# Kernel optimization log

Hardware: AMD Instinct MI355X
Metric: run time of the kernel (lower is better)

Reference implementation:

```python
import jax, jax.numpy as jnp
import numpy as np

B, S, P, D, H, L, DF, O = 8, 1024, 128, 256, 4, 4, 1024, 10
DH = D // H  # 64
EPS = 1e-5


def get_positional_embeddings(seq_len, d):
    i = np.arange(seq_len, dtype=np.float64)[:, None]
    j = np.arange(d, dtype=np.float64)[None, :]
    even = np.sin(i / 10000 ** (j / d))
    odd = np.cos(i / 10000 ** ((j - 1) / d))
    return jnp.asarray(np.where(j % 2 == 0, even, odd), dtype=jnp.float32)


def layernorm(x, g, b):
    m = jnp.mean(x, axis=-1, keepdims=True)
    v = jnp.mean(jnp.square(x - m), axis=-1, keepdims=True)
    return (x - m) * jax.lax.rsqrt(v + EPS) * g + b


def setup_inputs() -> dict:
    key = jax.random.key(0)
    ks = jax.random.split(key, 20)
    w = lambda k, shp: (jax.random.normal(k, shp, dtype=jnp.float32) * 0.02)
    return {
        "images": jax.random.normal(ks[0], (B, S, P), dtype=jnp.float32),
        "Wp": w(ks[1], (D, P)), "bp": jnp.zeros((D,), jnp.float32),
        "cls": jax.random.uniform(ks[2], (1, D), dtype=jnp.float32),
        "pos": get_positional_embeddings(S + 1, D),
        "ln1_g": jnp.ones((L, D), jnp.float32), "ln1_b": jnp.zeros((L, D), jnp.float32),
        "Wq": w(ks[3], (L, H, DH, DH)), "bq": jnp.zeros((L, H, DH), jnp.float32),
        "Wk": w(ks[4], (L, H, DH, DH)), "bk": jnp.zeros((L, H, DH), jnp.float32),
        "Wv": w(ks[5], (L, H, DH, DH)), "bv": jnp.zeros((L, H, DH), jnp.float32),
        "ln2_g": jnp.ones((L, D), jnp.float32), "ln2_b": jnp.zeros((L, D), jnp.float32),
        "W1": w(ks[6], (L, DF, D)), "b1": jnp.zeros((L, DF), jnp.float32),
        "W2": w(ks[7], (L, D, DF)), "b2": jnp.zeros((L, D), jnp.float32),
        "Wo": w(ks[8], (O, D)), "bo": jnp.zeros((O,), jnp.float32),
    }


def msa(x, Wq, bq, Wk, bk, Wv, bv):
    b, s, _ = x.shape
    xh = x.reshape(b, s, H, DH)  # split heads along feature dim
    # torch Linear: y = x @ W.T + b, per head
    q = jnp.einsum("bshd,hed->bhse", xh, Wq) + bq[None, :, None, :]
    k = jnp.einsum("bshd,hed->bhse", xh, Wk) + bk[None, :, None, :]
    v = jnp.einsum("bshd,hed->bhse", xh, Wv) + bv[None, :, None, :]
    scores = jnp.einsum("bhqd,bhkd->bhqk", q, k) / (DH ** 0.5)
    attn = jax.nn.softmax(scores, axis=-1)
    out = jnp.einsum("bhqk,bhkd->bhqd", attn, v)  # [b,h,s,dh]
    return out.transpose(0, 2, 1, 3).reshape(b, s, D)  # hstack heads


def reference(images, Wp, bp, cls, pos, ln1_g, ln1_b, Wq, bq, Wk, bk, Wv, bv,
              ln2_g, ln2_b, W1, b1, W2, b2, Wo, bo):
    tokens = jnp.einsum("bsp,dp->bsd", images, Wp) + bp
    x = jnp.concatenate([jnp.broadcast_to(cls[None], (B, 1, D)), tokens], axis=1)
    x = x + pos[None]
    for l in range(L):
        x = x + msa(layernorm(x, ln1_g[l], ln1_b[l]), Wq[l], bq[l], Wk[l], bk[l], Wv[l], bv[l])
        h = layernorm(x, ln2_g[l], ln2_b[l])
        h = jax.nn.gelu(jnp.einsum("bsd,fd->bsf", h, W1[l]) + b1[l], approximate=False)
        x = x + jnp.einsum("bsf,df->bsd", h, W2[l]) + b2[l]
    logits = x[:, 0] @ Wo.T + bo
    return jax.nn.softmax(logits, axis=-1)
```

## Files before the change

kernel.cpp:

```cpp
#include <hip/hip_runtime.h>
#include <hip/hip_bf16.h>
#include <cmath>

constexpr int B  = 8;
constexpr int S  = 1024;
constexpr int P  = 128;
constexpr int D  = 256;
constexpr int H  = 4;
constexpr int L  = 4;
constexpr int DF = 1024;
constexpr int O  = 10;
constexpr int DH = D / H;
constexpr int SP = S + 1;
constexpr int N  = B * SP;
constexpr int KVPAD = 1088;

typedef short bf16x8 __attribute__((ext_vector_type(8)));
typedef float f32x4 __attribute__((ext_vector_type(4)));
typedef float f32x16 __attribute__((ext_vector_type(16)));
typedef unsigned int u32;
typedef unsigned short u16;

static __device__ __forceinline__ u16 f2b(float f) {
    __hip_bfloat16 h = __float2bfloat16(f);
    u16 u; __builtin_memcpy(&u, &h, 2);
    return u;
}
static __device__ __forceinline__ float b2f(u16 u) {
    u32 uu = (u32)u << 16; float f; __builtin_memcpy(&f, &uu, 4);
    return f;
}
static __device__ __forceinline__ u32 pk2(float a, float b) {
    return (u32)f2b(a) | ((u32)f2b(b) << 16);
}
static __device__ __forceinline__ void gload_lds16(const void* g, void* l) {
    __builtin_amdgcn_global_load_lds((const __attribute__((address_space(1))) unsigned int*)g,
                                     (__attribute__((address_space(3))) unsigned int*)l, 16, 0, 0);
}

__global__ void cvt_all(const float* __restrict__ s0, u16* __restrict__ d0, int n0,
                        const float* __restrict__ s1, u16* __restrict__ d1, int n1,
                        const float* __restrict__ s2, u16* __restrict__ d2, int n2,
                        const float* __restrict__ s3, u16* __restrict__ d3, int n3) {
    int y = blockIdx.y;
    const float* s = y == 0 ? s0 : y == 1 ? s1 : y == 2 ? s2 : s3;
    u16* d = y == 0 ? d0 : y == 1 ? d1 : y == 2 ? d2 : d3;
    int n = y == 0 ? n0 : y == 1 ? n1 : y == 2 ? n2 : n3;
    int i = blockIdx.x * 256 + threadIdx.x;
    if (i < n) {
        float4 v = ((const float4*)s)[i];
        ushort4 o;
        o.x = f2b(v.x); o.y = f2b(v.y); o.z = f2b(v.z); o.w = f2b(v.w);
        ((ushort4*)d)[i] = o;
    }
}

__global__ void cls_kernel(const float* __restrict__ cls, const float* __restrict__ pos,
                           float* __restrict__ x) {
    int b = blockIdx.x, t = threadIdx.x;
    x[(size_t)b * SP * D + t] = cls[t] + pos[t];
}

__global__ void build_wqkv(const float* __restrict__ Wq, const float* __restrict__ bq,
                           const float* __restrict__ Wk, const float* __restrict__ bk,
                           const float* __restrict__ Wv, const float* __restrict__ bv,
                           u16* __restrict__ Wout, float* __restrict__ bout) {
    int r = blockIdx.x, l = blockIdx.y, c = threadIdx.x;
    int sec = r >> 8;
    int ef = r & 255, h = ef >> 6, e = ef & 63;
    const float* W  = sec == 0 ? Wq : sec == 1 ? Wk : Wv;
    const float* bi = sec == 0 ? bq : sec == 1 ? bk : bv;
    float scale = sec == 0 ? 0.125f * 1.4426950408889634f : 1.0f;
    float val = ((c >> 6) == h) ? W[(((size_t)l * H + h) * 64 + e) * 64 + (c & 63)] * scale : 0.f;
    Wout[((size_t)l * 768 + r) * 256 + c] = f2b(val);
    if (c == 0) bout[(size_t)l * 768 + r] = bi[((size_t)l * H + h) * 64 + e] * scale;
}

template <int EPI>
__global__ __launch_bounds__(256) void gemm_bf16(
        const u16* __restrict__ X, const u16* __restrict__ W,
        const float* __restrict__ bias, const float* __restrict__ pos,
        float* __restrict__ Yf, u16* __restrict__ Yb,
        int M, int F, int K, int kLen) {
    __shared__ u16 Al[2][64 * 64];
    __shared__ u16 Bl[2][128 * 64];
    const int t = threadIdx.x;
    const int m0 = blockIdx.y * 64, f0 = blockIdx.x * 128;
    const int w = t >> 6, l = t & 63;
    const int wm = w >> 1, wn = w & 1;
    const int q = l & 15, g = l >> 4;
    const int kOff = blockIdx.z * kLen;
    const int lr8 = l >> 3, lp = l & 7;

    f32x4 acc[2][4];
    const f32x4 zz = {0.f, 0.f, 0.f, 0.f};
#pragma unroll
    for (int i = 0; i < 2; ++i)
#pragma unroll
        for (int j = 0; j < 4; ++j) acc[i][j] = zz;

    auto stage = [&](int sb, int kbase) {
#pragma unroll
        for (int i = 0; i < 2; ++i) {
            int ca = w + 4 * i;
            int row = ca * 8 + lr8;
            int j = lp ^ (row & 7);
            gload_lds16(X + (size_t)(m0 + row) * K + kbase + j * 8, &Al[sb][ca * 512]);
        }
#pragma unroll
        for (int i = 0; i < 4; ++i) {
            int cb = w + 4 * i;
            int row = cb * 8 + lr8;
            int j = lp ^ (row & 7);
            gload_lds16(W + (size_t)(f0 + row) * K + kbase + j * 8, &Bl[sb][cb * 512]);
        }
    };

    const int nt = kLen / 64;
    stage(0, kOff);
    __syncthreads();
    int sb = 0;
    for (int ts = 0; ts < nt; ++ts) {
        if (ts + 1 < nt) stage(sb ^ 1, kOff + (ts + 1) * 64);
#pragma unroll
        for (int kk = 0; kk < 2; ++kk) {
            bf16x8 a[2], bfr[4];
#pragma unroll
            for (int fi = 0; fi < 2; ++fi) {
                int row = wm * 32 + fi * 16 + q;
                a[fi] = *(const bf16x8*)&Al[sb][row * 64 + (((kk * 4 + g) ^ (row & 7)) * 8)];
            }
#pragma unroll
            for (int fj = 0; fj < 4; ++fj) {
                int row = wn * 64 + fj * 16 + q;
                bfr[fj] = *(const bf16x8*)&Bl[sb][row * 64 + (((kk * 4 + g) ^ (row & 7)) * 8)];
            }
#pragma unroll
            for (int fi = 0; fi < 2; ++fi)
#pragma unroll
                for (int fj = 0; fj < 4; ++fj)
                    acc[fi][fj] = __builtin_amdgcn_mfma_f32_16x16x32_bf16(a[fi], bfr[fj], acc[fi][fj], 0, 0, 0);
        }
        __syncthreads();
        sb ^= 1;
    }

#pragma unroll
    for (int fi = 0; fi < 2; ++fi) {
#pragma unroll
        for (int r = 0; r < 4; ++r) {
            int m = m0 + wm * 32 + fi * 16 + g * 4 + r;
            if (m >= M) continue;
#pragma unroll
            for (int fj = 0; fj < 4; ++fj) {
                int f = f0 + wn * 64 + fj * 16 + q;
                float val = acc[fi][fj][r];
                if constexpr (EPI == 0) {
                    val += bias[f];
                    int s = m & 1023, bb = m >> 10;
                    size_t n = (size_t)bb * SP + s + 1;
                    Yf[n * D + f] = val + pos[(size_t)(s + 1) * D + f];
                } else if constexpr (EPI == 1) {
                    val += bias[f];
                    float gel = 0.5f * val * (1.0f + erff(val * 0.70710678118654752f));
                    Yb[(size_t)m * F + f] = f2b(gel);
                } else if constexpr (EPI == 2) {
                    val += bias[f];
                    Yf[(size_t)m * F + f] += val;
                } else if constexpr (EPI == 3) {
                    val += bias[f];
                    Yb[(size_t)m * F + f] = f2b(val);
                } else {
                    (Yf + (size_t)blockIdx.z * M * F)[(size_t)m * F + f] = val;
                }
            }
        }
    }
}

__global__ void transpose_v(const u16* __restrict__ qkv, u16* __restrict__ VTg) {
    __shared__ u16 tile[64][70];
    int bh = blockIdx.y, t0 = blockIdx.x * 64;
    int b = bh >> 2, h = bh & 3;
    int t = threadIdx.x;
    int r = t >> 3, c8 = (t & 7) * 8;
#pragma unroll
    for (int it = 0; it < 2; ++it) {
        int sp = t0 + it * 32 + r; if (sp > S) sp = S;
        uint4 v = *(const uint4*)(qkv + ((size_t)b * SP + sp) * 768 + 512 + h * 64 + c8);
        u32* dst = (u32*)&tile[it * 32 + r][c8];
        const u32* pv = (const u32*)&v;
#pragma unroll
        for (int k = 0; k < 4; ++k) dst[k] = pv[k];
    }
    __syncthreads();
#pragma unroll
    for (int it = 0; it < 2; ++it) {
        int d = it * 32 + (t >> 3);
        int spc = (t & 7) * 8;
        u16 tmp[8];
#pragma unroll
        for (int j = 0; j < 8; ++j) tmp[j] = tile[spc + j][d];
        *(uint4*)(VTg + ((size_t)bh * 64 + d) * KVPAD + t0 + spc) = *(const uint4*)tmp;
    }
}

__global__ void layernorm_bf16(const float* __restrict__ src,
                               const float* __restrict__ gw,
                               const float* __restrict__ bw,
                               u16* __restrict__ dst) {
    int row = blockIdx.x * 4 + (threadIdx.x >> 6);
    int l = threadIdx.x & 63;
    float4 v = *(const float4*)(src + (size_t)row * D + l * 4);
    float s = v.x + v.y + v.z + v.w;
    for (int off = 32; off; off >>= 1) s += __shfl_xor(s, off, 64);
    float mean = s * (1.0f / D);
    float dx0 = v.x - mean, dx1 = v.y - mean, dx2 = v.z - mean, dx3 = v.w - mean;
    float sq = dx0 * dx0 + dx1 * dx1 + dx2 * dx2 + dx3 * dx3;
    for (int off = 32; off; off >>= 1) sq += __shfl_xor(sq, off, 64);
    float rs = rsqrtf(sq * (1.0f / D) + 1e-5f);
    float4 gv = *(const float4*)(gw + l * 4);
    float4 bv = *(const float4*)(bw + l * 4);
    ushort4 o;
    o.x = f2b(dx0 * rs * gv.x + bv.x);
    o.y = f2b(dx1 * rs * gv.y + bv.y);
    o.z = f2b(dx2 * rs * gv.z + bv.z);
    o.w = f2b(dx3 * rs * gv.w + bv.w);
    *(ushort4*)(dst + (size_t)row * D + l * 4) = o;
}

__global__ __launch_bounds__(512, 4) void attn_stage(const u16* __restrict__ qkv,
                                                     const u16* __restrict__ VTg,
                                                     u16* __restrict__ opart,
                                                     float* __restrict__ lsum,
                                                     int nqt) {
    const int qg = blockIdx.x, bh = blockIdx.y, quarter = blockIdx.z;
    const int h4 = bh & 3, b = bh >> 2;
    const int t = threadIdx.x;
    const int wv = t >> 6, l = t & 63;
    const int col = l & 31, hh = l >> 5;

    __shared__ u16 Kl[5 * 64 * 64];
    __shared__ u16 Vl[5 * 64 * 64];

    const int kv_start = quarter * 256;
    const int kv_len = (quarter == 3) ? (SP - 768) : 256;
    const int ntiles = (kv_len + 63) >> 6;

    const int qt = qg * 8 + wv;
    const int q0w = qt * 32;

    bf16x8 qf[4];
    {
        int qr = q0w + col; if (qr > S) qr = S;
        const u16* qp = qkv + ((size_t)b * SP + qr) * 768 + h4 * 64 + hh * 8;
#pragma unroll
        for (int c = 0; c < 4; ++c) qf[c] = *(const bf16x8*)(qp + c * 16);
    }

    {
        const int rloc = wv * 8 + (l >> 3);
        const int j = (l & 7) ^ (((rloc >> 3) ^ rloc) & 7);
        for (int tt = 0; tt < ntiles; ++tt) {
            int krow = kv_start + tt * 64 + rloc; if (krow > S) krow = S;
            gload_lds16(qkv + ((size_t)b * SP + krow) * 768 + 256 + h4 * 64 + j * 8,
                        &Kl[(tt * 8 + wv) * 512]);
            gload_lds16(VTg + ((size_t)bh * 64 + rloc) * KVPAD + kv_start + tt * 64 + j * 8,
                        &Vl[(tt * 8 + wv) * 512]);
        }
    }
    __syncthreads();
    if (qt >= nqt) return;

    const int swA = ((col >> 3) ^ col) & 7;
    const int swB = swA ^ 4;

    f32x16 o0, o1;
#pragma unroll
    for (int r = 0; r < 16; ++r) { o0[r] = 0.f; o1[r] = 0.f; }
    float l_run = 0.f;

    for (int tile = 0; tile < ntiles; ++tile) {
        const int kv0 = tile * 64;
        const u16* Kt = &Kl[tile * 4096];
        const u16* Vt = &Vl[tile * 4096];

        f32x16 s0, s1;
#pragma unroll
        for (int r = 0; r < 16; ++r) { s0[r] = 0.f; s1[r] = 0.f; }
        __builtin_amdgcn_s_setprio(1);
#pragma unroll
        for (int c = 0; c < 4; ++c) {
            bf16x8 k0 = *(const bf16x8*)&Kt[col * 64 + (((2 * c + hh) ^ swA) * 8)];
            bf16x8 k1 = *(const bf16x8*)&Kt[(32 + col) * 64 + (((2 * c + hh) ^ swB) * 8)];
            s0 = __builtin_amdgcn_mfma_f32_32x32x16_bf16(k0, qf[c], s0, 0, 0, 0);
            s1 = __builtin_amdgcn_mfma_f32_32x32x16_bf16(k1, qf[c], s1, 0, 0, 0);
        }
        __builtin_amdgcn_s_setprio(0);

        float p[32];
#pragma unroll
        for (int r = 0; r < 16; ++r) { p[r] = s0[r]; p[16 + r] = s1[r]; }

        if (kv0 + 64 > kv_len) {
#pragma unroll
            for (int kvs = 0; kvs < 2; ++kvs)
#pragma unroll
                for (int r = 0; r < 16; ++r) {
                    int kvloc = kvs * 32 + (r & 3) + 8 * (r >> 2) + 4 * hh;
                    if (kv0 + kvloc >= kv_len) p[kvs * 16 + r] = -1e30f;
                }
        }

#pragma unroll
        for (int j = 0; j < 32; ++j) p[j] = exp2f(p[j]);
        {
            float t16[16];
#pragma unroll
            for (int j = 0; j < 16; ++j) t16[j] = p[2 * j] + p[2 * j + 1];
#pragma unroll
            for (int j = 0; j < 8; ++j) t16[j] = t16[j] + t16[j + 8];
#pragma unroll
            for (int j = 0; j < 4; ++j) t16[j] = t16[j] + t16[j + 4];
            l_run += (t16[0] + t16[1]) + (t16[2] + t16[3]);
        }

        __builtin_amdgcn_s_setprio(1);
#pragma unroll
        for (int kvs = 0; kvs < 2; ++kvs) {
            u32 pk[8];
#pragma unroll
            for (int i = 0; i < 8; ++i) pk[i] = pk2(p[kvs * 16 + 2 * i], p[kvs * 16 + 2 * i + 1]);
            u32 ex[4];
#pragma unroll
            for (int kk = 0; kk < 4; ++kk) {
                const int k = (kk < 2) ? kk : kk + 2;
                u32 send = hh ? pk[k] : pk[k + 2];
                ex[kk] = (u32)__shfl_xor((int)send, 32);
            }
#pragma unroll
            for (int cc = 0; cc < 2; ++cc) {
                union { u32 u[4]; bf16x8 v; } pa;
                u32 e0 = ex[cc * 2], e1 = ex[cc * 2 + 1];
                pa.u[0] = hh ? e0 : pk[4 * cc];
                pa.u[1] = hh ? e1 : pk[4 * cc + 1];
                pa.u[2] = hh ? pk[4 * cc + 2] : e0;
                pa.u[3] = hh ? pk[4 * cc + 3] : e1;
                int lch = kvs * 4 + cc * 2 + hh;
                bf16x8 v0 = *(const bf16x8*)&Vt[col * 64 + ((lch ^ swA) * 8)];
                bf16x8 v1 = *(const bf16x8*)&Vt[(32 + col) * 64 + ((lch ^ swB) * 8)];
                o0 = __builtin_amdgcn_mfma_f32_32x32x16_bf16(pa.v, v0, o0, 0, 0, 0);
                o1 = __builtin_amdgcn_mfma_f32_32x32x16_bf16(pa.v, v1, o1, 0, 0, 0);
            }
        }
        __builtin_amdgcn_s_setprio(0);
    }

    float l_full = l_run + __shfl_xor(l_run, 32);
    float inv = 1.0f / l_full;
    const size_t obase = ((size_t)quarter * 32 + bh) * SP;
#pragma unroll
    for (int r = 0; r < 16; ++r) {
        int qrow = (r & 3) + 8 * (r >> 2) + 4 * hh;
        float iv = __shfl(inv, qrow);
        int qq = q0w + qrow;
        if (qq < SP) {
            opart[(obase + qq) * 64 + col]      = f2b(o0[r] * iv);
            opart[(obase + qq) * 64 + 32 + col] = f2b(o1[r] * iv);
        }
    }
    if (l < 32) {
        int qq = q0w + l;
        if (qq < SP) lsum[obase + qq] = l_full;
    }
}

__global__ void combine_ln2(const u16* __restrict__ opart, const float* __restrict__ lsum,
                            const float* __restrict__ gw, const float* __restrict__ bw,
                            float* __restrict__ x, u16* __restrict__ lnb) {
    int row = blockIdx.x * 4 + (threadIdx.x >> 6);
    int l = threadIdx.x & 63;
    int b = row / SP, qq = row % SP;
    int h = l >> 4, d0 = (l * 4) & 63;
    int bh = b * 4 + h;
    float csum = 0.f, a0 = 0.f, a1 = 0.f, a2 = 0.f, a3 = 0.f;
#pragma unroll
    for (int i = 0; i < 4; ++i) {
        size_t idx = ((size_t)i * 32 + bh) * SP + qq;
        float c = lsum[idx];
        csum += c;
        ushort4 ov = *(const ushort4*)&opart[idx * 64 + d0];
        a0 += c * b2f(ov.x); a1 += c * b2f(ov.y); a2 += c * b2f(ov.z); a3 += c * b2f(ov.w);
    }
    float inv = 1.0f / csum;
    float4 xv = *(const float4*)(x + (size_t)row * D + l * 4);
    xv.x += a0 * inv; xv.y += a1 * inv; xv.z += a2 * inv; xv.w += a3 * inv;
    *(float4*)(x + (size_t)row * D + l * 4) = xv;

    float s = xv.x + xv.y + xv.z + xv.w;
    for (int off = 32; off; off >>= 1) s += __shfl_xor(s, off, 64);
    float mean = s * (1.0f / D);
    float dx0 = xv.x - mean, dx1 = xv.y - mean, dx2 = xv.z - mean, dx3 = xv.w - mean;
    float sq = dx0 * dx0 + dx1 * dx1 + dx2 * dx2 + dx3 * dx3;
    for (int off = 32; off; off >>= 1) sq += __shfl_xor(sq, off, 64);
    float rs = rsqrtf(sq * (1.0f / D) + 1e-5f);
    float4 gv = *(const float4*)(gw + l * 4);
    float4 bv = *(const float4*)(bw + l * 4);
    ushort4 o;
    o.x = f2b(dx0 * rs * gv.x + bv.x);
    o.y = f2b(dx1 * rs * gv.y + bv.y);
    o.z = f2b(dx2 * rs * gv.z + bv.z);
    o.w = f2b(dx3 * rs * gv.w + bv.w);
    *(ushort4*)(lnb + (size_t)row * D + l * 4) = o;
}

__global__ void combine2_ln1(const float* __restrict__ Pk, const float* __restrict__ b2,
                             const float* __restrict__ gw, const float* __restrict__ bw,
                             float* __restrict__ x, u16* __restrict__ lnb) {
    int row = blockIdx.x * 4 + (threadIdx.x >> 6);
    int l = threadIdx.x & 63;
    float4 p0 = ((const float4*)Pk)[(size_t)row * 64 + l];
    float4 p1 = ((const float4*)Pk)[(size_t)N * 64 + (size_t)row * 64 + l];
    float4 bv2 = *(const float4*)(b2 + l * 4);
    float4 xv = *(const float4*)(x + (size_t)row * D + l * 4);
    xv.x += p0.x + p1.x + bv2.x;
    xv.y += p0.y + p1.y + bv2.y;
    xv.z += p0.z + p1.z + bv2.z;
    xv.w += p0.w + p1.w + bv2.w;
    *(float4*)(x + (size_t)row * D + l * 4) = xv;

    float s = xv.x + xv.y + xv.z + xv.w;
    for (int off = 32; off; off >>= 1) s += __shfl_xor(s, off, 64);
    float mean = s * (1.0f / D);
    float dx0 = xv.x - mean, dx1 = xv.y - mean, dx2 = xv.z - mean, dx3 = xv.w - mean;
    float sq = dx0 * dx0 + dx1 * dx1 + dx2 * dx2 + dx3 * dx3;
    for (int off = 32; off; off >>= 1) sq += __shfl_xor(sq, off, 64);
    float rs = rsqrtf(sq * (1.0f / D) + 1e-5f);
    float4 gv = *(const float4*)(gw + l * 4);
    float4 bv = *(const float4*)(bw + l * 4);
    ushort4 o;
    o.x = f2b(dx0 * rs * gv.x + bv.x);
    o.y = f2b(dx1 * rs * gv.y + bv.y);
    o.z = f2b(dx2 * rs * gv.z + bv.z);
    o.w = f2b(dx3 * rs * gv.w + bv.w);
    *(ushort4*)(lnb + (size_t)row * D + l * 4) = o;
}

__global__ void combine_cls_ln2(const u16* __restrict__ opart, const float* __restrict__ lsum,
                                const float* __restrict__ x,
                                const float* __restrict__ gw, const float* __restrict__ bw,
                                float* __restrict__ x_cls, u16* __restrict__ lnb_cls) {
    int b = blockIdx.x * 4 + (threadIdx.x >> 6);
    int l = threadIdx.x & 63;
    int h = l >> 4, d0 = (l * 4) & 63;
    int bh = b * 4 + h;
    float csum = 0.f, a0 = 0.f, a1 = 0.f, a2 = 0.f, a3 = 0.f;
#pragma unroll
    for (int i = 0; i < 4; ++i) {
        size_t idx = ((size_t)i * 32 + bh) * SP;
        float c = lsum[idx];
        csum += c;
        ushort4 ov = *(const ushort4*)&opart[idx * 64 + d0];
        a0 += c * b2f(ov.x); a1 += c * b2f(ov.y); a2 += c * b2f(ov.z); a3 += c * b2f(ov.w);
    }
    float inv = 1.0f / csum;
    float4 xv = *(const float4*)(x + (size_t)b * SP * D + l * 4);
    xv.x += a0 * inv; xv.y += a1 * inv; xv.z += a2 * inv; xv.w += a3 * inv;
    *(float4*)(x_cls + (size_t)b * D + l * 4) = xv;

    float s = xv.x + xv.y + xv.z + xv.w;
    for (int off = 32; off; off >>= 1) s += __shfl_xor(s, off, 64);
    float mean = s * (1.0f / D);
    float dx0 = xv.x - mean, dx1 = xv.y - mean, dx2 = xv.z - mean, dx3 = xv.w - mean;
    float sq = dx0 * dx0 + dx1 * dx1 + dx2 * dx2 + dx3 * dx3;
    for (int off = 32; off; off >>= 1) sq += __shfl_xor(sq, off, 64);
    float rs = rsqrtf(sq * (1.0f / D) + 1e-5f);
    float4 gv = *(const float4*)(gw + l * 4);
    float4 bv = *(const float4*)(bw + l * 4);
    ushort4 o;
    o.x = f2b(dx0 * rs * gv.x + bv.x);
    o.y = f2b(dx1 * rs * gv.y + bv.y);
    o.z = f2b(dx2 * rs * gv.z + bv.z);
    o.w = f2b(dx3 * rs * gv.w + bv.w);
    *(ushort4*)(lnb_cls + (size_t)b * D + l * 4) = o;
}

__global__ void head_kernel(const float* __restrict__ xc,
                            const float* __restrict__ Wo,
                            const float* __restrict__ bo,
                            float* __restrict__ out) {
    __shared__ float logits[B][O];
    int t = threadIdx.x;
    if (t < B * O) {
        int b = t / O, o = t % O;
        const float* xr = xc + (size_t)b * D;
        float acc = bo[o];
        for (int d = 0; d < D; ++d) acc += xr[d] * Wo[(size_t)o * D + d];
        logits[b][o] = acc;
    }
    __syncthreads();
    if (t < B) {
        float mx = -1e30f;
        for (int o = 0; o < O; ++o) mx = fmaxf(mx, logits[t][o]);
        float s = 0.f, e[O];
        for (int o = 0; o < O; ++o) { e[o] = expf(logits[t][o] - mx); s += e[o]; }
        float inv = 1.0f / s;
        for (int o = 0; o < O; ++o) out[t * O + o] = e[o] * inv;
    }
}

extern "C" void kernel_launch(void* const* d_in, const int* in_sizes, int n_in,
                              void* d_out, int out_size, void* d_ws, size_t ws_size,
                              hipStream_t stream) {
    const float* images = (const float*)d_in[0];
    const float* Wp     = (const float*)d_in[1];
    const float* bp     = (const float*)d_in[2];
    const float* cls    = (const float*)d_in[3];
    const float* pos    = (const float*)d_in[4];
    const float* ln1_g  = (const float*)d_in[5];
    const float* ln1_b  = (const float*)d_in[6];
    const float* Wq     = (const float*)d_in[7];
    const float* bq     = (const float*)d_in[8];
    const float* Wk     = (const float*)d_in[9];
    const float* bk     = (const float*)d_in[10];
    const float* Wv     = (const float*)d_in[11];
    const float* bv     = (const float*)d_in[12];
    const float* ln2_g  = (const float*)d_in[13];
    const float* ln2_b  = (const float*)d_in[14];
    const float* W1     = (const float*)d_in[15];
    const float* b1     = (const float*)d_in[16];
    const float* W2     = (const float*)d_in[17];
    const float* b2     = (const float*)d_in[18];
    const float* Wo     = (const float*)d_in[19];
    const float* bo     = (const float*)d_in[20];
    float* out = (float*)d_out;

    auto align256 = [](size_t v) { return (v + 255) & ~(size_t)255; };
    char* p = (char*)d_ws;
    float* x      = (float*)p; p += align256((size_t)N * D * 4);
    u16* lnb      = (u16*)p;   p += align256((size_t)N * D * 2);
    u16* qkvbuf   = (u16*)p;   p += align256((size_t)(N + 64) * 768 * 2);
    char* midop   = p;         p += align256((size_t)N * DF * 2);
    float* Pk     = (float*)p; p += align256((size_t)2 * N * D * 4);
    float* lsum   = (float*)p; p += align256((size_t)4 * 32 * SP * 4);
    u16* VTg      = (u16*)p;   p += align256((size_t)32 * 64 * KVPAD * 2);
    u16* imgb     = (u16*)p;   p += align256((size_t)B * S * P * 2);
    u16* Wpb      = (u16*)p;   p += align256((size_t)D * P * 2);
    u16* W1b      = (u16*)p;   p += align256((size_t)L * DF * D * 2);
    u16* W2b      = (u16*)p;   p += align256((size_t)L * D * DF * 2);
    u16* Wqkvb    = (u16*)p;   p += align256((size_t)L * 768 * 256 * 2);
    float* bqkvf  = (float*)p; p += align256((size_t)L * 768 * 4);
    float* x_cls  = (float*)p; p += align256((size_t)64 * D * 4);
    u16* lnb_cls  = (u16*)p;   p += align256((size_t)64 * D * 2);
    u16* mid_cls  = (u16*)p;   p += align256((size_t)64 * DF * 2);
    u16* mid      = (u16*)midop;
    u16* opart    = (u16*)midop;

    cvt_all<<<dim3(1024, 4), 256, 0, stream>>>(
        images, imgb, B * S * P / 4,
        Wp, Wpb, D * P / 4,
        W1, W1b, L * DF * D / 4,
        W2, W2b, L * D * DF / 4);
    build_wqkv<<<dim3(768, L), 256, 0, stream>>>(Wq, bq, Wk, bk, Wv, bv, Wqkvb, bqkvf);

    gemm_bf16<0><<<dim3(2, 128, 1), 256, 0, stream>>>(
        imgb, Wpb, bp, pos, x, nullptr, B * S, D, P, P);
    cls_kernel<<<B, D, 0, stream>>>(cls, pos, x);
    layernorm_bf16<<<N / 4, 256, 0, stream>>>(x, ln1_g, ln1_b, lnb);

    for (int l = 0; l < 3; ++l) {
        gemm_bf16<3><<<dim3(6, 129, 1), 256, 0, stream>>>(
            lnb, Wqkvb + (size_t)l * 768 * 256, bqkvf + (size_t)l * 768,
            nullptr, nullptr, qkvbuf, N, 768, D, D);
        transpose_v<<<dim3(17, 32), 256, 0, stream>>>(qkvbuf, VTg);
        attn_stage<<<dim3(5, 32, 4), 512, 0, stream>>>(qkvbuf, VTg, opart, lsum, 33);
        combine_ln2<<<N / 4, 256, 0, stream>>>(opart, lsum, ln2_g + l * D, ln2_b + l * D, x, lnb);
        gemm_bf16<1><<<dim3(8, 129, 1), 256, 0, stream>>>(
            lnb, W1b + (size_t)l * DF * D, b1 + (size_t)l * DF,
            nullptr, nullptr, mid, N, DF, D, D);
        gemm_bf16<4><<<dim3(2, 129, 2), 256, 0, stream>>>(
            mid, W2b + (size_t)l * D * DF, nullptr, nullptr, Pk, nullptr, N, D, DF, DF / 2);
        combine2_ln1<<<N / 4, 256, 0, stream>>>(Pk, b2 + (size_t)l * D,
                                                ln1_g + (l + 1) * D, ln1_b + (l + 1) * D, x, lnb);
    }

    {
        const int l = 3;
        gemm_bf16<3><<<dim3(6, 129, 1), 256, 0, stream>>>(
            lnb, Wqkvb + (size_t)l * 768 * 256, bqkvf + (size_t)l * 768,
            nullptr, nullptr, qkvbuf, N, 768, D, D);
        transpose_v<<<dim3(17, 32), 256, 0, stream>>>(qkvbuf, VTg);
        attn_stage<<<dim3(1, 32, 4), 512, 0, stream>>>(qkvbuf, VTg, opart, lsum, 1);
        combine_cls_ln2<<<2, 256, 0, stream>>>(opart, lsum, x, ln2_g + l * D, ln2_b + l * D,
                                               x_cls, lnb_cls);
        gemm_bf16<1><<<dim3(8, 1, 1), 256, 0, stream>>>(
            lnb_cls, W1b + (size_t)l * DF * D, b1 + (size_t)l * DF,
            nullptr, nullptr, mid_cls, B, DF, D, D);
        gemm_bf16<2><<<dim3(2, 1, 1), 256, 0, stream>>>(
            mid_cls, W2b + (size_t)l * D * DF, b2 + (size_t)l * D,
            nullptr, x_cls, nullptr, B, D, DF, DF);
    }

    head_kernel<<<1, 256, 0, stream>>>(x_cls, Wo, bo, out);
}
```

Before: 357.5 us.

## Split attention KV into nine chunks with smaller 256-thread blocks

The attention kernel now splits each sequence's keys into nine chunks of 128 (the last holding the single leftover key) instead of four of 256. Blocks shrink from 8 to 4 waves, so the grid grows from 5x32x4 to 9x32x9 and each block uses less LDS, aiming for more parallelism and occupancy on the GPU. The combine kernels now merge nine partial outputs per row, and opart gets its own buffer instead of aliasing the MLP mid buffer. In exchange this adds more partial-output memory traffic, more redundant Q loads, and a nearly empty ninth split.

```diff
diff --git a/kernel.cpp b/kernel.cpp
--- a/kernel.cpp
+++ b/kernel.cpp
@@ -14,6 +14,7 @@
 constexpr int SP = S + 1;
 constexpr int N  = B * SP;
 constexpr int KVPAD = 1088;
+constexpr int NSPLIT = 9;
 
 typedef short bf16x8 __attribute__((ext_vector_type(8)));
 typedef float f32x4 __attribute__((ext_vector_type(4)));
@@ -229,25 +230,25 @@
     *(ushort4*)(dst + (size_t)row * D + l * 4) = o;
 }
 
-__global__ __launch_bounds__(512, 4) void attn_stage(const u16* __restrict__ qkv,
+__global__ __launch_bounds__(256, 5) void attn_stage(const u16* __restrict__ qkv,
                                                      const u16* __restrict__ VTg,
                                                      u16* __restrict__ opart,
                                                      float* __restrict__ lsum,
                                                      int nqt) {
-    const int qg = blockIdx.x, bh = blockIdx.y, quarter = blockIdx.z;
+    const int qg = blockIdx.x, bh = blockIdx.y, split = blockIdx.z;
     const int h4 = bh & 3, b = bh >> 2;
     const int t = threadIdx.x;
     const int wv = t >> 6, l = t & 63;
     const int col = l & 31, hh = l >> 5;
 
-    __shared__ u16 Kl[5 * 64 * 64];
-    __shared__ u16 Vl[5 * 64 * 64];
-
-    const int kv_start = quarter * 256;
-    const int kv_len = (quarter == 3) ? (SP - 768) : 256;
-    const int ntiles = (kv_len + 63) >> 6;
-
-    const int qt = qg * 8 + wv;
+    __shared__ u16 Kl[2 * 64 * 64];
+    __shared__ u16 Vl[2 * 64 * 64];
+
+    const int kv_start = split * 128;
+    const int kv_len = (split == 8) ? 1 : 128;
+    const int ntiles = (split == 8) ? 1 : 2;
+
+    const int qt = qg * 4 + wv;
     const int q0w = qt * 32;
 
     bf16x8 qf[4];
@@ -259,14 +260,19 @@
     }
 
     {
-        const int rloc = wv * 8 + (l >> 3);
-        const int j = (l & 7) ^ (((rloc >> 3) ^ rloc) & 7);
+        const int lr8 = l >> 3, lp = l & 7;
         for (int tt = 0; tt < ntiles; ++tt) {
-            int krow = kv_start + tt * 64 + rloc; if (krow > S) krow = S;
-            gload_lds16(qkv + ((size_t)b * SP + krow) * 768 + 256 + h4 * 64 + j * 8,
-                        &Kl[(tt * 8 + wv) * 512]);
-            gload_lds16(VTg + ((size_t)bh * 64 + rloc) * KVPAD + kv_start + tt * 64 + j * 8,
-                        &Vl[(tt * 8 + wv) * 512]);
+#pragma unroll
+            for (int i = 0; i < 2; ++i) {
+                int slab = wv * 2 + i;
+                int rloc = slab * 8 + lr8;
+                int j = lp ^ (((rloc >> 3) ^ rloc) & 7);
+                int krow = kv_start + tt * 64 + rloc; if (krow > S) krow = S;
+                gload_lds16(qkv + ((size_t)b * SP + krow) * 768 + 256 + h4 * 64 + j * 8,
+                            &Kl[(tt * 8 + slab) * 512]);
+                gload_lds16(VTg + ((size_t)bh * 64 + rloc) * KVPAD + kv_start + tt * 64 + j * 8,
+                            &Vl[(tt * 8 + slab) * 512]);
+            }
         }
     }
     __syncthreads();
@@ -358,7 +364,7 @@
 
     float l_full = l_run + __shfl_xor(l_run, 32);
     float inv = 1.0f / l_full;
-    const size_t obase = ((size_t)quarter * 32 + bh) * SP;
+    const size_t obase = ((size_t)split * 32 + bh) * SP;
 #pragma unroll
     for (int r = 0; r < 16; ++r) {
         int qrow = (r & 3) + 8 * (r >> 2) + 4 * hh;
@@ -385,7 +391,7 @@
     int bh = b * 4 + h;
     float csum = 0.f, a0 = 0.f, a1 = 0.f, a2 = 0.f, a3 = 0.f;
 #pragma unroll
-    for (int i = 0; i < 4; ++i) {
+    for (int i = 0; i < NSPLIT; ++i) {
         size_t idx = ((size_t)i * 32 + bh) * SP + qq;
         float c = lsum[idx];
         csum += c;
@@ -456,7 +462,7 @@
     int bh = b * 4 + h;
     float csum = 0.f, a0 = 0.f, a1 = 0.f, a2 = 0.f, a3 = 0.f;
 #pragma unroll
-    for (int i = 0; i < 4; ++i) {
+    for (int i = 0; i < NSPLIT; ++i) {
         size_t idx = ((size_t)i * 32 + bh) * SP;
         float c = lsum[idx];
         csum += c;
@@ -540,9 +546,10 @@
     float* x      = (float*)p; p += align256((size_t)N * D * 4);
     u16* lnb      = (u16*)p;   p += align256((size_t)N * D * 2);
     u16* qkvbuf   = (u16*)p;   p += align256((size_t)(N + 64) * 768 * 2);
-    char* midop   = p;         p += align256((size_t)N * DF * 2);
+    u16* mid      = (u16*)p;   p += align256((size_t)N * DF * 2);
     float* Pk     = (float*)p; p += align256((size_t)2 * N * D * 4);
-    float* lsum   = (float*)p; p += align256((size_t)4 * 32 * SP * 4);
+    float* lsum   = (float*)p; p += align256((size_t)NSPLIT * 32 * SP * 4);
+    u16* opart    = (u16*)p;   p += align256((size_t)NSPLIT * 32 * SP * 64 * 2);
     u16* VTg      = (u16*)p;   p += align256((size_t)32 * 64 * KVPAD * 2);
     u16* imgb     = (u16*)p;   p += align256((size_t)B * S * P * 2);
     u16* Wpb      = (u16*)p;   p += align256((size_t)D * P * 2);
@@ -553,8 +560,6 @@
     float* x_cls  = (float*)p; p += align256((size_t)64 * D * 4);
     u16* lnb_cls  = (u16*)p;   p += align256((size_t)64 * D * 2);
     u16* mid_cls  = (u16*)p;   p += align256((size_t)64 * DF * 2);
-    u16* mid      = (u16*)midop;
-    u16* opart    = (u16*)midop;
 
     cvt_all<<<dim3(1024, 4), 256, 0, stream>>>(
         images, imgb, B * S * P / 4,
@@ -573,7 +578,7 @@
             lnb, Wqkvb + (size_t)l * 768 * 256, bqkvf + (size_t)l * 768,
             nullptr, nullptr, qkvbuf, N, 768, D, D);
         transpose_v<<<dim3(17, 32), 256, 0, stream>>>(qkvbuf, VTg);
-        attn_stage<<<dim3(5, 32, 4), 512, 0, stream>>>(qkvbuf, VTg, opart, lsum, 33);
+        attn_stage<<<dim3(9, 32, NSPLIT), 256, 0, stream>>>(qkvbuf, VTg, opart, lsum, 33);
         combine_ln2<<<N / 4, 256, 0, stream>>>(opart, lsum, ln2_g + l * D, ln2_b + l * D, x, lnb);
         gemm_bf16<1><<<dim3(8, 129, 1), 256, 0, stream>>>(
             lnb, W1b + (size_t)l * DF * D, b1 + (size_t)l * DF,
@@ -590,7 +595,7 @@
             lnb, Wqkvb + (size_t)l * 768 * 256, bqkvf + (size_t)l * 768,
             nullptr, nullptr, qkvbuf, N, 768, D, D);
         transpose_v<<<dim3(17, 32), 256, 0, stream>>>(qkvbuf, VTg);
-        attn_stage<<<dim3(1, 32, 4), 512, 0, stream>>>(qkvbuf, VTg, opart, lsum, 1);
+        attn_stage<<<dim3(1, 32, NSPLIT), 256, 0, stream>>>(qkvbuf, VTg, opart, lsum, 1);
         combine_cls_ln2<<<2, 256, 0, stream>>>(opart, lsum, x, ln2_g + l * D, ln2_b + l * D,
                                                x_cls, lnb_cls);
         gemm_bf16<1><<<dim3(8, 1, 1), 256, 0, stream>>>(
```

Result: slower. 437.9 us (+22.5%).

## Compute QKV per head with block-diagonal GEMM over K=64 instead of dense K=256

Applied to the files above, without the earlier changes.

The QKV projection used a dense 768x256 weight that was three-quarters zeros because of the per-head block-diagonal structure. It now runs a per-head GEMM (grid z = head) over K=64, producing a head-major qkvh buffer of shape [H][N][192]. The attention and V-transpose kernels are updated to read this layout. The GEMM kernel is generalised with separate X leading dimension, weight stride and per-z weight offset, and clamps weight rows for the 192-wide output, which leaves some idle lanes in the 128-column tiles.

```diff
diff --git a/kernel.cpp b/kernel.cpp
--- a/kernel.cpp
+++ b/kernel.cpp
@@ -65,15 +65,15 @@
                            const float* __restrict__ Wk, const float* __restrict__ bk,
                            const float* __restrict__ Wv, const float* __restrict__ bv,
                            u16* __restrict__ Wout, float* __restrict__ bout) {
-    int r = blockIdx.x, l = blockIdx.y, c = threadIdx.x;
-    int sec = r >> 8;
-    int ef = r & 255, h = ef >> 6, e = ef & 63;
+    int r = blockIdx.x, l = blockIdx.y;
+    int h = threadIdx.x >> 6, c = threadIdx.x & 63;
+    int sec = r >> 6, e = r & 63;
     const float* W  = sec == 0 ? Wq : sec == 1 ? Wk : Wv;
     const float* bi = sec == 0 ? bq : sec == 1 ? bk : bv;
     float scale = sec == 0 ? 0.125f * 1.4426950408889634f : 1.0f;
-    float val = ((c >> 6) == h) ? W[(((size_t)l * H + h) * 64 + e) * 64 + (c & 63)] * scale : 0.f;
-    Wout[((size_t)l * 768 + r) * 256 + c] = f2b(val);
-    if (c == 0) bout[(size_t)l * 768 + r] = bi[((size_t)l * H + h) * 64 + e] * scale;
+    Wout[(((size_t)(l * 4 + h)) * 192 + r) * 64 + c] =
+        f2b(W[(((size_t)l * H + h) * 64 + e) * 64 + c] * scale);
+    if (c == 0) bout[((size_t)(l * 4 + h)) * 192 + r] = bi[((size_t)l * H + h) * 64 + e] * scale;
 }
 
 template <int EPI>
@@ -81,7 +81,7 @@
         const u16* __restrict__ X, const u16* __restrict__ W,
         const float* __restrict__ bias, const float* __restrict__ pos,
         float* __restrict__ Yf, u16* __restrict__ Yb,
-        int M, int F, int K, int kLen) {
+        int M, int F, int kLen, int ldx, int kw, size_t wz) {
     __shared__ u16 Al[2][64 * 64];
     __shared__ u16 Bl[2][128 * 64];
     const int t = threadIdx.x;
@@ -99,29 +99,32 @@
 #pragma unroll
         for (int j = 0; j < 4; ++j) acc[i][j] = zz;
 
-    auto stage = [&](int sb, int kbase) {
+    auto stage = [&](int sb, int ts) {
+        const int xk = kOff + ts * 64;
+        const size_t wk = (size_t)blockIdx.z * wz + (size_t)ts * 64;
 #pragma unroll
         for (int i = 0; i < 2; ++i) {
             int ca = w + 4 * i;
             int row = ca * 8 + lr8;
             int j = lp ^ (row & 7);
-            gload_lds16(X + (size_t)(m0 + row) * K + kbase + j * 8, &Al[sb][ca * 512]);
+            gload_lds16(X + (size_t)(m0 + row) * ldx + xk + j * 8, &Al[sb][ca * 512]);
         }
 #pragma unroll
         for (int i = 0; i < 4; ++i) {
             int cb = w + 4 * i;
             int row = cb * 8 + lr8;
+            int rw = f0 + row; if (rw > F - 1) rw = F - 1;
             int j = lp ^ (row & 7);
-            gload_lds16(W + (size_t)(f0 + row) * K + kbase + j * 8, &Bl[sb][cb * 512]);
+            gload_lds16(W + (size_t)rw * kw + wk + j * 8, &Bl[sb][cb * 512]);
         }
     };
 
     const int nt = kLen / 64;
-    stage(0, kOff);
+    stage(0, 0);
     __syncthreads();
     int sb = 0;
     for (int ts = 0; ts < nt; ++ts) {
-        if (ts + 1 < nt) stage(sb ^ 1, kOff + (ts + 1) * 64);
+        if (ts + 1 < nt) stage(sb ^ 1, ts + 1);
 #pragma unroll
         for (int kk = 0; kk < 2; ++kk) {
             bf16x8 a[2], bfr[4];
@@ -170,15 +173,20 @@
                 } else if constexpr (EPI == 3) {
                     val += bias[f];
                     Yb[(size_t)m * F + f] = f2b(val);
+                } else if constexpr (EPI == 4) {
+                    (Yf + (size_t)blockIdx.z * M * F)[(size_t)m * F + f] = val;
                 } else {
-                    (Yf + (size_t)blockIdx.z * M * F)[(size_t)m * F + f] = val;
+                    if (f < F) {
+                        val += bias[blockIdx.z * 192 + f];
+                        Yb[((size_t)blockIdx.z * N + m) * 192 + f] = f2b(val);
+                    }
                 }
             }
         }
     }
 }
 
-__global__ void transpose_v(const u16* __restrict__ qkv, u16* __restrict__ VTg) {
+__global__ void transpose_v(const u16* __restrict__ qkvh, u16* __restrict__ VTg) {
     __shared__ u16 tile[64][70];
     int bh = blockIdx.y, t0 = blockIdx.x * 64;
     int b = bh >> 2, h = bh & 3;
@@ -187,7 +195,7 @@
 #pragma unroll
     for (int it = 0; it < 2; ++it) {
         int sp = t0 + it * 32 + r; if (sp > S) sp = S;
-        uint4 v = *(const uint4*)(qkv + ((size_t)b * SP + sp) * 768 + 512 + h * 64 + c8);
+        uint4 v = *(const uint4*)(qkvh + ((size_t)h * N + (size_t)b * SP + sp) * 192 + 128 + c8);
         u32* dst = (u32*)&tile[it * 32 + r][c8];
         const u32* pv = (const u32*)&v;
 #pragma unroll
@@ -229,7 +237,7 @@
     *(ushort4*)(dst + (size_t)row * D + l * 4) = o;
 }
 
-__global__ __launch_bounds__(512, 4) void attn_stage(const u16* __restrict__ qkv,
+__global__ __launch_bounds__(512, 4) void attn_stage(const u16* __restrict__ qkvh,
                                                      const u16* __restrict__ VTg,
                                                      u16* __restrict__ opart,
                                                      float* __restrict__ lsum,
@@ -250,10 +258,12 @@
     const int qt = qg * 8 + wv;
     const int q0w = qt * 32;
 
+    const u16* qbase = qkvh + (size_t)h4 * N * 192;
+
     bf16x8 qf[4];
     {
         int qr = q0w + col; if (qr > S) qr = S;
-        const u16* qp = qkv + ((size_t)b * SP + qr) * 768 + h4 * 64 + hh * 8;
+        const u16* qp = qbase + ((size_t)b * SP + qr) * 192 + hh * 8;
 #pragma unroll
         for (int c = 0; c < 4; ++c) qf[c] = *(const bf16x8*)(qp + c * 16);
     }
@@ -263,7 +273,7 @@
         const int j = (l & 7) ^ (((rloc >> 3) ^ rloc) & 7);
         for (int tt = 0; tt < ntiles; ++tt) {
             int krow = kv_start + tt * 64 + rloc; if (krow > S) krow = S;
-            gload_lds16(qkv + ((size_t)b * SP + krow) * 768 + 256 + h4 * 64 + j * 8,
+            gload_lds16(qbase + ((size_t)b * SP + krow) * 192 + 64 + j * 8,
                         &Kl[(tt * 8 + wv) * 512]);
             gload_lds16(VTg + ((size_t)bh * 64 + rloc) * KVPAD + kv_start + tt * 64 + j * 8,
                         &Vl[(tt * 8 + wv) * 512]);
@@ -539,7 +549,7 @@
     char* p = (char*)d_ws;
     float* x      = (float*)p; p += align256((size_t)N * D * 4);
     u16* lnb      = (u16*)p;   p += align256((size_t)N * D * 2);
-    u16* qkvbuf   = (u16*)p;   p += align256((size_t)(N + 64) * 768 * 2);
+    u16* qkvh     = (u16*)p;   p += align256((size_t)H * N * 192 * 2);
     char* midop   = p;         p += align256((size_t)N * DF * 2);
     float* Pk     = (float*)p; p += align256((size_t)2 * N * D * 4);
     float* lsum   = (float*)p; p += align256((size_t)4 * 32 * SP * 4);
@@ -548,8 +558,8 @@
     u16* Wpb      = (u16*)p;   p += align256((size_t)D * P * 2);
     u16* W1b      = (u16*)p;   p += align256((size_t)L * DF * D * 2);
     u16* W2b      = (u16*)p;   p += align256((size_t)L * D * DF * 2);
-    u16* Wqkvb    = (u16*)p;   p += align256((size_t)L * 768 * 256 * 2);
-    float* bqkvf  = (float*)p; p += align256((size_t)L * 768 * 4);
+    u16* Wqkvb    = (u16*)p;   p += align256((size_t)L * H * 192 * 64 * 2);
+    float* bqkvf  = (float*)p; p += align256((size_t)L * H * 192 * 4);
     float* x_cls  = (float*)p; p += align256((size_t)64 * D * 4);
     u16* lnb_cls  = (u16*)p;   p += align256((size_t)64 * D * 2);
     u16* mid_cls  = (u16*)p;   p += align256((size_t)64 * DF * 2);
@@ -561,44 +571,45 @@
         Wp, Wpb, D * P / 4,
         W1, W1b, L * DF * D / 4,
         W2, W2b, L * D * DF / 4);
-    build_wqkv<<<dim3(768, L), 256, 0, stream>>>(Wq, bq, Wk, bk, Wv, bv, Wqkvb, bqkvf);
+    build_wqkv<<<dim3(192, L), 256, 0, stream>>>(Wq, bq, Wk, bk, Wv, bv, Wqkvb, bqkvf);
 
     gemm_bf16<0><<<dim3(2, 128, 1), 256, 0, stream>>>(
-        imgb, Wpb, bp, pos, x, nullptr, B * S, D, P, P);
+        imgb, Wpb, bp, pos, x, nullptr, B * S, D, P, P, P, (size_t)P);
     cls_kernel<<<B, D, 0, stream>>>(cls, pos, x);
     layernorm_bf16<<<N / 4, 256, 0, stream>>>(x, ln1_g, ln1_b, lnb);
 
     for (int l = 0; l < 3; ++l) {
-        gemm_bf16<3><<<dim3(6, 129, 1), 256, 0, stream>>>(
-            lnb, Wqkvb + (size_t)l * 768 * 256, bqkvf + (size_t)l * 768,
-            nullptr, nullptr, qkvbuf, N, 768, D, D);
-        transpose_v<<<dim3(17, 32), 256, 0, stream>>>(qkvbuf, VTg);
-        attn_stage<<<dim3(5, 32, 4), 512, 0, stream>>>(qkvbuf, VTg, opart, lsum, 33);
+        gemm_bf16<5><<<dim3(2, 129, H), 256, 0, stream>>>(
+            lnb, Wqkvb + (size_t)l * H * 192 * 64, bqkvf + (size_t)l * H * 192,
+            nullptr, nullptr, qkvh, N, 192, 64, 256, 64, (size_t)192 * 64);
+        transpose_v<<<dim3(17, 32), 256, 0, stream>>>(qkvh, VTg);
+        attn_stage<<<dim3(5, 32, 4), 512, 0, stream>>>(qkvh, VTg, opart, lsum, 33);
         combine_ln2<<<N / 4, 256, 0, stream>>>(opart, lsum, ln2_g + l * D, ln2_b + l * D, x, lnb);
         gemm_bf16<1><<<dim3(8, 129, 1), 256, 0, stream>>>(
             lnb, W1b + (size_t)l * DF * D, b1 + (size_t)l * DF,
-            nullptr, nullptr, mid, N, DF, D, D);
+            nullptr, nullptr, mid, N, DF, D, D, D, (size_t)D);
         gemm_bf16<4><<<dim3(2, 129, 2), 256, 0, stream>>>(
-            mid, W2b + (size_t)l * D * DF, nullptr, nullptr, Pk, nullptr, N, D, DF, DF / 2);
+            mid, W2b + (size_t)l * D * DF, nullptr, nullptr, Pk, nullptr,
+            N, D, DF / 2, DF, DF, (size_t)DF / 2);
         combine2_ln1<<<N / 4, 256, 0, stream>>>(Pk, b2 + (size_t)l * D,
                                                 ln1_g + (l + 1) * D, ln1_b + (l + 1) * D, x, lnb);
     }
 
     {
         const int l = 3;
-        gemm_bf16<3><<<dim3(6, 129, 1), 256, 0, stream>>>(
-            lnb, Wqkvb + (size_t)l * 768 * 256, bqkvf + (size_t)l * 768,
-            nullptr, nullptr, qkvbuf, N, 768, D, D);
-        transpose_v<<<dim3(17, 32), 256, 0, stream>>>(qkvbuf, VTg);
-        attn_stage<<<dim3(1, 32, 4), 512, 0, stream>>>(qkvbuf, VTg, opart, lsum, 1);
+        gemm_bf16<5><<<dim3(2, 129, H), 256, 0, stream>>>(
+            lnb, Wqkvb + (size_t)l * H * 192 * 64, bqkvf + (size_t)l * H * 192,
+            nullptr, nullptr, qkvh, N, 192, 64, 256, 64, (size_t)192 * 64);
+        transpose_v<<<dim3(17, 32), 256, 0, stream>>>(qkvh, VTg);
+        attn_stage<<<dim3(1, 32, 4), 512, 0, stream>>>(qkvh, VTg, opart, lsum, 1);
         combine_cls_ln2<<<2, 256, 0, stream>>>(opart, lsum, x, ln2_g + l * D, ln2_b + l * D,
                                                x_cls, lnb_cls);
         gemm_bf16<1><<<dim3(8, 1, 1), 256, 0, stream>>>(
             lnb_cls, W1b + (size_t)l * DF * D, b1 + (size_t)l * DF,
-            nullptr, nullptr, mid_cls, B, DF, D, D);
+            nullptr, nullptr, mid_cls, B, DF, D, D, D, (size_t)D);
         gemm_bf16<2><<<dim3(2, 1, 1), 256, 0, stream>>>(
             mid_cls, W2b + (size_t)l * D * DF, b2 + (size_t)l * D,
-            nullptr, x_cls, nullptr, B, D, DF, DF);
+            nullptr, x_cls, nullptr, B, D, DF, DF, DF, (size_t)DF);
     }
 
     head_kernel<<<1, 256, 0, stream>>>(x_cls, Wo, bo, out);
```

Result: slower. 374.2 us (+4.7%).
